# Performance work log

Hardware: AMD Instinct MI355X
Metric: run time of the kernel (lower is better)

## Reference

```python
import jax, jax.numpy as jnp
import numpy as np

B, HH, WW, C, HEADS = 8, 56, 56, 384, 6
DIM_OUT = 384


def _upsample2x_bilinear(x):
    # x: [..., m, n] -> [..., 2m, 2n]; matches torch F.interpolate bilinear align_corners=False
    m, n = x.shape[-2], x.shape[-1]
    def coords(inn):
        c = (jnp.arange(2 * inn) + 0.5) / 2.0 - 0.5
        c = jnp.clip(c, 0.0, inn - 1)
        i0 = jnp.floor(c).astype(jnp.int32)
        i1 = jnp.minimum(i0 + 1, inn - 1)
        return i0, i1, (c - i0).astype(x.dtype)
    i0, i1, wy = coords(m)
    j0, j1, wx = coords(n)
    rows = x[..., i0, :] * (1 - wy)[:, None] + x[..., i1, :] * wy[:, None]
    return rows[..., :, j0] * (1 - wx) + rows[..., :, j1] * wx


def setup_inputs() -> dict:
    key = jax.random.key(0)
    ks = jax.random.split(key, 12)
    inp = {
        'x': jax.random.normal(ks[0], (B, HH * WW, C), jnp.float32),
        'res_attn': jax.random.normal(ks[1], (B, HEADS, (HH // 4) * (WW // 4), (HH // 2) * (WW // 2)), jnp.float32),
        'conv_q_w': jax.random.normal(ks[2], (C, 1, 3, 3), jnp.float32) * 0.05,
        'ln_g': jnp.ones((C,), jnp.float32),
        'ln_b': jnp.zeros((C,), jnp.float32),
        'wq': jax.random.normal(ks[3], (DIM_OUT, C), jnp.float32) * 0.02,
        'wk': jax.random.normal(ks[4], (DIM_OUT, C), jnp.float32) * 0.02,
        'wv': jax.random.normal(ks[5], (DIM_OUT, C), jnp.float32) * 0.02,
        'w_proj': jax.random.normal(ks[6], (DIM_OUT, DIM_OUT), jnp.float32) * 0.02,
        'b_proj': jnp.zeros((DIM_OUT,), jnp.float32),
        'w_fuse': jax.random.normal(ks[7], (HEADS, 2 * HEADS, 1, 1), jnp.float32) * 0.1,
        'b_fuse': jnp.zeros((HEADS,), jnp.float32),
        'h': HH,
        'w': WW,
    }
    return inp


def reference(x, res_attn, conv_q_w, ln_g, ln_b, wq, wk, wv, w_proj, b_proj, w_fuse, b_fuse, h, w):
    Bz, _, Cc = x.shape
    heads = w_fuse.shape[0]
    xi = x.transpose(0, 2, 1).reshape(Bz, Cc, h, w)  # b c h w
    # conv_proj_q: depthwise conv k3 s2 p1 (no bias), then LayerNorm
    q = jax.lax.conv_general_dilated(
        xi, conv_q_w, (2, 2), ((1, 1), (1, 1)),
        dimension_numbers=('NCHW', 'OIHW', 'NCHW'), feature_group_count=Cc)
    hq, wq2 = q.shape[2], q.shape[3]
    q = q.reshape(Bz, Cc, hq * wq2).transpose(0, 2, 1)  # b t c
    mu = q.mean(-1, keepdims=True)
    var = ((q - mu) ** 2).mean(-1, keepdims=True)
    q = (q - mu) / jnp.sqrt(var + 1e-5) * ln_g + ln_b
    # conv_proj_k/v: avg pool k2 s2 p0
    kv = xi.reshape(Bz, Cc, h // 2, 2, w // 2, 2).mean(axis=(3, 5))
    kv = kv.reshape(Bz, Cc, (h // 2) * (w // 2)).transpose(0, 2, 1)  # b t c
    dim_out = wq.shape[0]
    dh = dim_out // heads
    def split(t):
        return t.reshape(Bz, t.shape[1], heads, dh).transpose(0, 2, 1, 3)
    qh = split(q @ wq.T)
    kh = split(kv @ wk.T)
    vh = split(kv @ wv.T)
    scale = dim_out ** -0.5
    attn_score = jnp.einsum('bhlk,bhtk->bhlt', qh, kh) * scale  # [B,H,L,T]
    sh, sw = h // 4, w // 4
    a = res_attn.shape[-1]
    rx = res_attn[:, :, :sh * sw, :]
    rx = rx.reshape(Bz * heads, sh * sw, a).transpose(0, 2, 1).reshape(Bz * heads, a, sh, sw)
    rx = _upsample2x_bilinear(rx)  # (b h) a 2sh 2sw
    rx = rx.reshape(Bz, heads, a, 4 * sh * sw).transpose(0, 1, 3, 2)  # b h L a
    cat = jnp.concatenate([attn_score, rx], axis=1)  # [B, 2H, L, T]
    attn_score = jnp.einsum('bclt,oc->bolt', cat, w_fuse[:, :, 0, 0]) + b_fuse[None, :, None, None]
    attn = jax.nn.softmax(attn_score, axis=-1)
    out = jnp.einsum('bhlt,bhtv->bhlv', attn, vh)
    out = out.transpose(0, 2, 1, 3).reshape(Bz, -1, dim_out)
    return out @ w_proj.T + b_proj
```

## Files before the change

### kernel.cpp

```cpp
#include <hip/hip_runtime.h>

typedef unsigned int uint;
typedef unsigned short ushort_t;
typedef short bf16x8 __attribute__((ext_vector_type(8)));
typedef float f32x4 __attribute__((ext_vector_type(4)));

__device__ __forceinline__ ushort_t f2bf(float f) {
  uint u = __builtin_bit_cast(uint, f);
  u += 0x7fffu + ((u >> 16) & 1u);
  return (ushort_t)(u >> 16);
}
__device__ __forceinline__ float bf2f(ushort_t s) {
  return __builtin_bit_cast(float, (uint)s << 16);
}
__device__ __forceinline__ float bflo(uint u) { return __builtin_bit_cast(float, u << 16); }
__device__ __forceinline__ float bfhi(uint u) { return __builtin_bit_cast(float, u & 0xffff0000u); }
__device__ __forceinline__ bf16x8 ld_frag(const ushort_t* p) {
  return __builtin_bit_cast(bf16x8, *(const uint4*)p);
}

__global__ __launch_bounds__(384) void k_prep(
    const float* __restrict__ x, const float* __restrict__ wc,
    const float* __restrict__ g, const float* __restrict__ bb,
    ushort_t* __restrict__ qout, ushort_t* __restrict__ kvout)
{
  const int b  = blockIdx.x / 784;
  const int t  = blockIdx.x % 784;
  const int oy = t / 28, ox = t % 28;
  const int c  = threadIdx.x;
  const float* xb = x + (size_t)b * 3136 * 384 + c;
  float tap[9];
  #pragma unroll
  for (int ky = 0; ky < 3; ky++) {
    const int iy = 2 * oy - 1 + ky;
    #pragma unroll
    for (int kx = 0; kx < 3; kx++) {
      const int ix = 2 * ox - 1 + kx;
      tap[ky * 3 + kx] = (iy >= 0 && iy < 56 && ix >= 0 && ix < 56)
                         ? xb[(size_t)(iy * 56 + ix) * 384] : 0.f;
    }
  }
  float acc = 0.f;
  #pragma unroll
  for (int k = 0; k < 9; k++) acc += wc[c * 9 + k] * tap[k];
  const float pool = (tap[4] + tap[5] + tap[7] + tap[8]) * 0.25f;

  float s = acc, s2 = acc * acc;
  #pragma unroll
  for (int off = 32; off >= 1; off >>= 1) {
    s  += __shfl_xor(s,  off);
    s2 += __shfl_xor(s2, off);
  }
  __shared__ float ps[6], ps2[6];
  if ((c & 63) == 0) { ps[c >> 6] = s; ps2[c >> 6] = s2; }
  __syncthreads();
  float S = 0.f, S2 = 0.f;
  #pragma unroll
  for (int i = 0; i < 6; i++) { S += ps[i]; S2 += ps2[i]; }
  const float mu  = S * (1.f / 384.f);
  const float var = S2 * (1.f / 384.f) - mu * mu;
  const float inv = rsqrtf(var + 1e-5f);
  const size_t o = ((size_t)b * 784 + t) * 384 + c;
  qout[o]  = f2bf((acc - mu) * inv * g[c] + bb[c]);
  kvout[o] = f2bf(pool);
}

__global__ __launch_bounds__(256) void k_wcvt(
    const float* __restrict__ a, const float* __restrict__ b,
    const float* __restrict__ c, const float* __restrict__ d,
    ushort_t* __restrict__ oa, ushort_t* __restrict__ ob,
    ushort_t* __restrict__ oc, ushort_t* __restrict__ od)
{
  const int i = blockIdx.x * 256 + threadIdx.x;
  if (i < 147456) {
    oa[i] = f2bf(a[i]); ob[i] = f2bf(b[i]);
    oc[i] = f2bf(c[i]); od[i] = f2bf(d[i]);
  }
}

__global__ __launch_bounds__(256) void k_rcmix(
    const float* __restrict__ ra, const float* __restrict__ w_fuse,
    ushort_t* __restrict__ RC)
{
  const int tid = threadIdx.x;
  const int b = blockIdx.x / 196, lc = blockIdx.x % 196;
  __shared__ float w2[36];
  if (tid < 36) w2[tid] = w_fuse[(tid / 6) * 12 + 6 + (tid % 6)];
  __syncthreads();
  const float* rab = ra + ((size_t)b * 6 * 196 + lc) * 784;
  ushort_t* RCb = RC + ((size_t)b * 6 * 196 + lc) * 784;
  for (int t = tid; t < 784; t += 256) {
    float U[6];
    #pragma unroll
    for (int c = 0; c < 6; c++) U[c] = rab[(size_t)c * 153664 + t];
    #pragma unroll
    for (int o = 0; o < 6; o++) {
      float v = 0.f;
      #pragma unroll
      for (int c = 0; c < 6; c++) v += w2[o * 6 + c] * U[c];
      RCb[(size_t)o * 153664 + t] = f2bf(v);
    }
  }
}

template<int MODE>
__global__ __launch_bounds__(256) void k_gemm(
    const ushort_t* __restrict__ X, const ushort_t* __restrict__ W,
    const float* __restrict__ bias, void* __restrict__ Y)
{
  __shared__ ushort_t As[128][40];
  __shared__ ushort_t Bs[128][40];
  const int tid = threadIdx.x, w = tid >> 6, lane = tid & 63;
  const int quad = lane >> 4, r = lane & 15;
  const int m0 = blockIdx.y * 128, n0 = blockIdx.x * 128;
  const int wm = w >> 1, wn = w & 1;
  const int lr = tid >> 2, lc = (tid & 3) << 3;
  const ushort_t* xp = X + (size_t)(m0 + lr) * 384 + lc;
  const ushort_t* wp = W + (size_t)(n0 + lr) * 384 + lc;
  f32x4 acc[4][4] = {};
  for (int k0 = 0; k0 < 384; k0 += 32) {
    __syncthreads();
    *(uint4*)&As[lr][lc]      = *(const uint4*)(xp + k0);
    *(uint4*)&As[lr + 64][lc] = *(const uint4*)(xp + (size_t)64 * 384 + k0);
    *(uint4*)&Bs[lr][lc]      = *(const uint4*)(wp + k0);
    *(uint4*)&Bs[lr + 64][lc] = *(const uint4*)(wp + (size_t)64 * 384 + k0);
    __syncthreads();
    bf16x8 af[4], bf_[4];
    #pragma unroll
    for (int mt = 0; mt < 4; mt++) af[mt]  = *(const bf16x8*)&As[wm * 64 + mt * 16 + r][quad * 8];
    #pragma unroll
    for (int nt = 0; nt < 4; nt++) bf_[nt] = *(const bf16x8*)&Bs[wn * 64 + nt * 16 + r][quad * 8];
    #pragma unroll
    for (int mt = 0; mt < 4; mt++)
      #pragma unroll
      for (int nt = 0; nt < 4; nt++)
        acc[mt][nt] = __builtin_amdgcn_mfma_f32_16x16x32_bf16(af[mt], bf_[nt], acc[mt][nt], 0, 0, 0);
  }
  #pragma unroll
  for (int mt = 0; mt < 4; mt++) {
    #pragma unroll
    for (int nt = 0; nt < 4; nt++) {
      #pragma unroll
      for (int i = 0; i < 4; i++) {
        const int row = m0 + wm * 64 + mt * 16 + quad * 4 + i;
        const int col = n0 + wn * 64 + nt * 16 + r;
        const float v = acc[mt][nt][i];
        if constexpr (MODE == 2) ((float*)Y)[(size_t)row * 384 + col] = v + bias[col];
        else                     ((ushort_t*)Y)[(size_t)row * 384 + col] = f2bf(v);
      }
    }
  }
}

__global__ __launch_bounds__(256) void k_gemmT(
    const ushort_t* __restrict__ W, const ushort_t* __restrict__ X,
    ushort_t* __restrict__ Vt)
{
  __shared__ ushort_t As[128][40];
  __shared__ ushort_t Bs[128][40];
  const int tid = threadIdx.x, w = tid >> 6, lane = tid & 63;
  const int quad = lane >> 4, r = lane & 15;
  const int m0 = blockIdx.y * 128, n0 = blockIdx.x * 128;
  const int wm = w >> 1, wn = w & 1;
  const int lr = tid >> 2, lc = (tid & 3) << 3;
  const ushort_t* ap = W + (size_t)(m0 + lr) * 384 + lc;
  const ushort_t* bp = X + (size_t)(n0 + lr) * 384 + lc;
  f32x4 acc[4][4] = {};
  for (int k0 = 0; k0 < 384; k0 += 32) {
    __syncthreads();
    *(uint4*)&As[lr][lc]      = *(const uint4*)(ap + k0);
    *(uint4*)&As[lr + 64][lc] = *(const uint4*)(ap + (size_t)64 * 384 + k0);
    *(uint4*)&Bs[lr][lc]      = *(const uint4*)(bp + k0);
    *(uint4*)&Bs[lr + 64][lc] = *(const uint4*)(bp + (size_t)64 * 384 + k0);
    __syncthreads();
    bf16x8 af[4], bf_[4];
    #pragma unroll
    for (int mt = 0; mt < 4; mt++) af[mt]  = *(const bf16x8*)&As[wm * 64 + mt * 16 + r][quad * 8];
    #pragma unroll
    for (int nt = 0; nt < 4; nt++) bf_[nt] = *(const bf16x8*)&Bs[wn * 64 + nt * 16 + r][quad * 8];
    #pragma unroll
    for (int mt = 0; mt < 4; mt++)
      #pragma unroll
      for (int nt = 0; nt < 4; nt++)
        acc[mt][nt] = __builtin_amdgcn_mfma_f32_16x16x32_bf16(af[mt], bf_[nt], acc[mt][nt], 0, 0, 0);
  }
  #pragma unroll
  for (int mt = 0; mt < 4; mt++) {
    #pragma unroll
    for (int nt = 0; nt < 4; nt++) {
      #pragma unroll
      for (int i = 0; i < 4; i++) {
        const int d   = m0 + wm * 64 + mt * 16 + quad * 4 + i;
        const int tok = n0 + wn * 64 + nt * 16 + r;
        const int b = tok / 784, tt = tok % 784;
        Vt[((size_t)b * 384 + d) * 784 + tt] = f2bf(acc[mt][nt][i]);
      }
    }
  }
}

__global__ __launch_bounds__(256, 3) void k_fattn(
    const ushort_t* __restrict__ Qb, const ushort_t* __restrict__ Kb,
    const ushort_t* __restrict__ Vt, const ushort_t* __restrict__ RC,
    const float* __restrict__ w_fuse, const float* __restrict__ b_fuse,
    float* __restrict__ Op, float2* __restrict__ MS)
{
  __shared__ char smem[27648];
  ushort_t* Ssc_ = (ushort_t*)smem;
  ushort_t* Pl_  = (ushort_t*)(smem + 13824);
  float*    stage = (float*)smem;
  #define SSC(h, l, t) Ssc_[(((h) * 16 + (l)) * 72) + (t)]
  #define PL(h, l, t)  Pl_[(((h) * 16 + (l)) * 72) + (t)]
  __shared__ float m_st[6][16], s_st[6][16], a_st[6][16];
  __shared__ float w1[36], bfu[6];

  const int tid  = threadIdx.x;
  const int w    = tid >> 6, lane = tid & 63;
  const int quad = lane >> 4, r = lane & 15;
  const int b    = blockIdx.x & 7;
  const int m0   = (blockIdx.x >> 3) * 16;
  const int s    = blockIdx.y;
  const int tile0 = (s == 0) ? 0 : (3 * s + 1);
  const int tileN = (s == 0) ? 4 : 3;
  const float scale = 0.05103103630798288f;

  if (tid < 36) w1[tid] = w_fuse[(tid / 6) * 12 + (tid % 6)] * scale;
  if (tid < 6)  bfu[tid] = b_fuse[tid];
  if (tid < 96) { (&m_st[0][0])[tid] = -1e30f; (&s_st[0][0])[tid] = 0.f; }

  const ushort_t* qrow = Qb + ((size_t)(b * 784 + m0 + r)) * 384 + quad * 8;
  bf16x8 qf[6][2];
  #pragma unroll
  for (int h = 0; h < 6; h++) {
    qf[h][0] = ld_frag(qrow + h * 64);
    qf[h][1] = ld_frag(qrow + h * 64 + 32);
  }

  const int bl_l = tid >> 4, tq = tid & 15;
  const int L = m0 + bl_l;
  const int Yc = L / 28, Xc = L % 28;
  const float cy = fminf(fmaxf((float)Yc * 0.5f - 0.25f, 0.f), 13.f);
  const float cx = fminf(fmaxf((float)Xc * 0.5f - 0.25f, 0.f), 13.f);
  const int y0 = (int)cy, y1 = min(y0 + 1, 13);
  const int x0 = (int)cx, x1 = min(x0 + 1, 13);
  const float fy = cy - (float)y0, fx = cx - (float)x0;
  const float w00 = (1.f - fy) * (1.f - fx), w01 = (1.f - fy) * fx;
  const float w10 = fy * (1.f - fx),         w11 = fy * fx;
  const int q00 = (y0 * 14 + x0) * 784, q01 = (y0 * 14 + x1) * 784;
  const int q10 = (y1 * 14 + x0) * 784, q11 = (y1 * 14 + x1) * 784;
  const ushort_t* RCb = RC + (size_t)b * 6 * 153664;

  const size_t kbase  = (size_t)b * 784 * 384;
  const size_t vtbase = (size_t)b * 384 * 784;

  f32x4 oacc[6] = {};

  for (int ii = 0; ii < tileN; ii++) {
    const int t0 = (tile0 + ii) * 64;

    {
      const int tA = min(t0 + w * 16 + r, 783);
      const ushort_t* krow = Kb + kbase + (size_t)tA * 384 + quad * 8;
      #pragma unroll
      for (int h = 0; h < 6; h++) {
        f32x4 sc = {};
        sc = __builtin_amdgcn_mfma_f32_16x16x32_bf16(qf[h][0], ld_frag(krow + h * 64),      sc, 0, 0, 0);
        sc = __builtin_amdgcn_mfma_f32_16x16x32_bf16(qf[h][1], ld_frag(krow + h * 64 + 32), sc, 0, 0, 0);
        #pragma unroll
        for (int i = 0; i < 4; i++)
          SSC(h, quad * 4 + i, w * 16 + r) = f2bf(sc[i]);
      }
    }
    __syncthreads();

    {
      const int t4 = t0 + tq * 4;
      float F[6][4];
      #pragma unroll
      for (int o = 0; o < 6; o++) {
        const ushort_t* rco = RCb + (size_t)o * 153664 + t4;
        const uint2 u00 = *(const uint2*)(rco + q00);
        const uint2 u01 = *(const uint2*)(rco + q01);
        const uint2 u10 = *(const uint2*)(rco + q10);
        const uint2 u11 = *(const uint2*)(rco + q11);
        F[o][0] = bfu[o] + w00 * bflo(u00.x) + w01 * bflo(u01.x) + w10 * bflo(u10.x) + w11 * bflo(u11.x);
        F[o][1] = bfu[o] + w00 * bfhi(u00.x) + w01 * bfhi(u01.x) + w10 * bfhi(u10.x) + w11 * bfhi(u11.x);
        F[o][2] = bfu[o] + w00 * bflo(u00.y) + w01 * bflo(u01.y) + w10 * bflo(u10.y) + w11 * bflo(u11.y);
        F[o][3] = bfu[o] + w00 * bfhi(u00.y) + w01 * bfhi(u01.y) + w10 * bfhi(u10.y) + w11 * bfhi(u11.y);
      }
      #pragma unroll
      for (int c = 0; c < 6; c++) {
        const uint2 sv = *(const uint2*)&SSC(c, bl_l, tq * 4);
        const float s0 = bflo(sv.x), s1 = bfhi(sv.x);
        const float s2 = bflo(sv.y), s3 = bfhi(sv.y);
        #pragma unroll
        for (int o = 0; o < 6; o++) {
          const float wv = w1[o * 6 + c];
          F[o][0] += wv * s0; F[o][1] += wv * s1;
          F[o][2] += wv * s2; F[o][3] += wv * s3;
        }
      }
      #pragma unroll
      for (int j = 0; j < 4; j++) {
        if (t4 + j >= 784) {
          #pragma unroll
          for (int o = 0; o < 6; o++) F[o][j] = -1e30f;
        }
      }
      #pragma unroll
      for (int o = 0; o < 6; o++) {
        float mx = fmaxf(fmaxf(F[o][0], F[o][1]), fmaxf(F[o][2], F[o][3]));
        #pragma unroll
        for (int off = 8; off >= 1; off >>= 1) mx = fmaxf(mx, __shfl_xor(mx, off));
        const float m_old = m_st[o][bl_l];
        const float nm = fmaxf(m_old, mx);
        const float al = __expf(m_old - nm);
        float p0 = __expf(F[o][0] - nm), p1 = __expf(F[o][1] - nm);
        float p2 = __expf(F[o][2] - nm), p3 = __expf(F[o][3] - nm);
        float sm = p0 + p1 + p2 + p3;
        #pragma unroll
        for (int off = 8; off >= 1; off >>= 1) sm += __shfl_xor(sm, off);
        const uint lo = (uint)f2bf(p0) | ((uint)f2bf(p1) << 16);
        const uint hi = (uint)f2bf(p2) | ((uint)f2bf(p3) << 16);
        *(uint2*)&PL(o, bl_l, tq * 4) = uint2{lo, hi};
        if (tq == 0) {
          m_st[o][bl_l] = nm;
          s_st[o][bl_l] = s_st[o][bl_l] * al + sm;
          a_st[o][bl_l] = al;
        }
      }
    }
    __syncthreads();

    #pragma unroll
    for (int o = 0; o < 6; o++) {
      const f32x4 al4 = *(const f32x4*)&a_st[o][quad * 4];
      oacc[o] *= al4;
      const bf16x8 pa0 = *(const bf16x8*)&PL(o, r, quad * 8);
      const bf16x8 pa1 = *(const bf16x8*)&PL(o, r, quad * 8 + 32);
      const ushort_t* vrow = Vt + vtbase + (size_t)(o * 64 + w * 16 + r) * 784 + t0 + quad * 8;
      oacc[o] = __builtin_amdgcn_mfma_f32_16x16x32_bf16(pa0, ld_frag(vrow),      oacc[o], 0, 0, 0);
      oacc[o] = __builtin_amdgcn_mfma_f32_16x16x32_bf16(pa1, ld_frag(vrow + 32), oacc[o], 0, 0, 0);
    }
    __syncthreads();
  }

  #pragma unroll
  for (int o = 0; o < 6; o++)
    #pragma unroll
    for (int i = 0; i < 4; i++)
      stage[(quad * 4 + i) * 392 + o * 64 + w * 16 + r] = oacc[o][i];
  __syncthreads();
  const size_t prow = (size_t)s * 6272 + (size_t)b * 784 + m0;
  #pragma unroll
  for (int j = 0; j < 6; j++) {
    const int idx = tid + j * 256;
    const int row = idx / 96, c4 = idx % 96;
    *(float4*)&Op[(prow + row) * 384 + c4 * 4] = *(const float4*)&stage[row * 392 + c4 * 4];
  }
  if (tid < 96) {
    const int l = tid / 6, o = tid % 6;
    MS[(prow + l) * 6 + o] = float2{m_st[o][l], s_st[o][l]};
  }
  #undef SSC
  #undef PL
}

__global__ __launch_bounds__(256) void k_comb(
    const float* __restrict__ Op, const float2* __restrict__ MS,
    ushort_t* __restrict__ O)
{
  const int idx = blockIdx.x * 256 + threadIdx.x;
  const int row = idx / 384, col = idx % 384, o = col >> 6;
  float2 ms[4];
  #pragma unroll
  for (int s = 0; s < 4; s++) ms[s] = MS[((size_t)s * 6272 + row) * 6 + o];
  float m = fmaxf(fmaxf(ms[0].x, ms[1].x), fmaxf(ms[2].x, ms[3].x));
  float S = 0.f, acc = 0.f;
  #pragma unroll
  for (int s = 0; s < 4; s++) {
    const float e = __expf(ms[s].x - m);
    S   += ms[s].y * e;
    acc += Op[((size_t)s * 6272 + row) * 384 + col] * e;
  }
  O[(size_t)row * 384 + col] = f2bf(acc / S);
}

extern "C" void kernel_launch(void* const* d_in, const int* in_sizes, int n_in,
                              void* d_out, int out_size, void* d_ws, size_t ws_size,
                              hipStream_t stream)
{
  const float* x        = (const float*)d_in[0];
  const float* res_attn = (const float*)d_in[1];
  const float* conv_w   = (const float*)d_in[2];
  const float* ln_g     = (const float*)d_in[3];
  const float* ln_b     = (const float*)d_in[4];
  const float* wq       = (const float*)d_in[5];
  const float* wk       = (const float*)d_in[6];
  const float* wv       = (const float*)d_in[7];
  const float* w_proj   = (const float*)d_in[8];
  const float* b_proj   = (const float*)d_in[9];
  const float* w_fuse   = (const float*)d_in[10];
  const float* b_fuse   = (const float*)d_in[11];
  float* out = (float*)d_out;

  const size_t NE  = (size_t)8 * 784 * 384;
  const size_t NW  = 147456;
  const size_t NRC = (size_t)8 * 6 * 196 * 784;
  ushort_t* q_ln_b = (ushort_t*)d_ws;
  ushort_t* kv_b   = q_ln_b + NE;
  ushort_t* Qb     = kv_b + NE;
  ushort_t* Kb     = Qb + NE;
  ushort_t* Vt     = Kb + NE;
  ushort_t* Opre   = Vt + NE + 64;
  ushort_t* wqb    = Opre + NE;
  ushort_t* wkb    = wqb + NW;
  ushort_t* wvb    = wkb + NW;
  ushort_t* wpb    = wvb + NW;
  ushort_t* RC     = wpb + NW;
  float*    Op     = (float*)(RC + NRC + 64);
  float2*   MS     = (float2*)(Op + 4 * NE);

  k_prep <<<dim3(8 * 784), dim3(384), 0, stream>>>(x, conv_w, ln_g, ln_b, q_ln_b, kv_b);
  k_wcvt <<<dim3(576),     dim3(256), 0, stream>>>(wq, wk, wv, w_proj, wqb, wkb, wvb, wpb);
  k_rcmix<<<dim3(8 * 196), dim3(256), 0, stream>>>(res_attn, w_fuse, RC);

  k_gemm<0><<<dim3(3, 49), dim3(256), 0, stream>>>(q_ln_b, wqb, nullptr, Qb);
  k_gemm<0><<<dim3(3, 49), dim3(256), 0, stream>>>(kv_b,   wkb, nullptr, Kb);
  k_gemmT  <<<dim3(49, 3), dim3(256), 0, stream>>>(wvb, kv_b, Vt);

  k_fattn<<<dim3(392, 4), dim3(256), 0, stream>>>(Qb, Kb, Vt, RC, w_fuse, b_fuse, Op, MS);
  k_comb <<<dim3(9408),   dim3(256), 0, stream>>>(Op, MS, Opre);

  k_gemm<2><<<dim3(3, 49), dim3(256), 0, stream>>>(Opre, wpb, b_proj, out);
}
```

Before: 354.2 us.

## Precompute upsampled residual mix and drop split-K attention combine

```diff
diff --git a/kernel.cpp b/kernel.cpp
--- a/kernel.cpp
+++ b/kernel.cpp
@@ -24,8 +24,8 @@
     const float* __restrict__ g, const float* __restrict__ bb,
     ushort_t* __restrict__ qout, ushort_t* __restrict__ kvout)
 {
-  const int b  = blockIdx.x / 784;
-  const int t  = blockIdx.x % 784;
+  const int b  = blockIdx.x & 7;
+  const int t  = blockIdx.x >> 3;
   const int oy = t / 28, ox = t % 28;
   const int c  = threadIdx.x;
   const float* xb = x + (size_t)b * 3136 * 384 + c;
@@ -78,27 +78,45 @@
   }
 }
 
-__global__ __launch_bounds__(256) void k_rcmix(
+__global__ __launch_bounds__(256) void k_resmix(
     const float* __restrict__ ra, const float* __restrict__ w_fuse,
-    ushort_t* __restrict__ RC)
+    const float* __restrict__ b_fuse, ushort_t* __restrict__ R)
 {
   const int tid = threadIdx.x;
-  const int b = blockIdx.x / 196, lc = blockIdx.x % 196;
-  __shared__ float w2[36];
+  const int b = blockIdx.x & 7, L = blockIdx.x >> 3;
+  __shared__ float w2[36], bfu[6];
   if (tid < 36) w2[tid] = w_fuse[(tid / 6) * 12 + 6 + (tid % 6)];
+  if (tid < 6)  bfu[tid] = b_fuse[tid];
   __syncthreads();
-  const float* rab = ra + ((size_t)b * 6 * 196 + lc) * 784;
-  ushort_t* RCb = RC + ((size_t)b * 6 * 196 + lc) * 784;
+
+  const int Yc = L / 28, Xc = L % 28;
+  const float cy = fminf(fmaxf((float)Yc * 0.5f - 0.25f, 0.f), 13.f);
+  const float cx = fminf(fmaxf((float)Xc * 0.5f - 0.25f, 0.f), 13.f);
+  const int y0 = (int)cy, y1 = min(y0 + 1, 13);
+  const int x0 = (int)cx, x1 = min(x0 + 1, 13);
+  const float fy = cy - (float)y0, fx = cx - (float)x0;
+  const float w00 = (1.f - fy) * (1.f - fx), w01 = (1.f - fy) * fx;
+  const float w10 = fy * (1.f - fx),         w11 = fy * fx;
+  const int p00 = (y0 * 14 + x0) * 784, p01 = (y0 * 14 + x1) * 784;
+  const int p10 = (y1 * 14 + x0) * 784, p11 = (y1 * 14 + x1) * 784;
+
+  const float* rab = ra + (size_t)b * 6 * 153664;
+  ushort_t* Rrow = R + ((size_t)(b * 784 + L) * 6) * 784;
+
   for (int t = tid; t < 784; t += 256) {
     float U[6];
     #pragma unroll
-    for (int c = 0; c < 6; c++) U[c] = rab[(size_t)c * 153664 + t];
+    for (int c = 0; c < 6; c++) {
+      const float* rc = rab + (size_t)c * 153664;
+      U[c] = w00 * rc[p00 + t] + w01 * rc[p01 + t]
+           + w10 * rc[p10 + t] + w11 * rc[p11 + t];
+    }
     #pragma unroll
     for (int o = 0; o < 6; o++) {
-      float v = 0.f;
+      float v = bfu[o];
       #pragma unroll
       for (int c = 0; c < 6; c++) v += w2[o * 6 + c] * U[c];
-      RCb[(size_t)o * 153664 + t] = f2bf(v);
+      Rrow[(size_t)o * 784 + t] = f2bf(v);
     }
   }
 }
@@ -199,36 +217,31 @@
   }
 }
 
-__global__ __launch_bounds__(256, 3) void k_fattn(
+__global__ __launch_bounds__(128, 2) void k_fattn(
     const ushort_t* __restrict__ Qb, const ushort_t* __restrict__ Kb,
-    const ushort_t* __restrict__ Vt, const ushort_t* __restrict__ RC,
-    const float* __restrict__ w_fuse, const float* __restrict__ b_fuse,
-    float* __restrict__ Op, float2* __restrict__ MS)
-{
-  __shared__ char smem[27648];
-  ushort_t* Ssc_ = (ushort_t*)smem;
-  ushort_t* Pl_  = (ushort_t*)(smem + 13824);
-  float*    stage = (float*)smem;
-  #define SSC(h, l, t) Ssc_[(((h) * 16 + (l)) * 72) + (t)]
-  #define PL(h, l, t)  Pl_[(((h) * 16 + (l)) * 72) + (t)]
-  __shared__ float m_st[6][16], s_st[6][16], a_st[6][16];
-  __shared__ float w1[36], bfu[6];
+    const ushort_t* __restrict__ Vt, const ushort_t* __restrict__ R,
+    const float* __restrict__ w_fuse, ushort_t* __restrict__ O)
+{
+  __shared__ ushort_t Ssc[6][16][72];
+  __shared__ ushort_t Pl[6][16][72];
+  __shared__ float m_st[6][8], s_st[6][8];
+  __shared__ float a_st[6][16];
+  __shared__ float w1[36];
 
   const int tid  = threadIdx.x;
   const int w    = tid >> 6, lane = tid & 63;
   const int quad = lane >> 4, r = lane & 15;
   const int b    = blockIdx.x & 7;
-  const int m0   = (blockIdx.x >> 3) * 16;
-  const int s    = blockIdx.y;
-  const int tile0 = (s == 0) ? 0 : (3 * s + 1);
-  const int tileN = (s == 0) ? 4 : 3;
+  const int m0   = (blockIdx.x >> 3) * 8;
   const float scale = 0.05103103630798288f;
 
   if (tid < 36) w1[tid] = w_fuse[(tid / 6) * 12 + (tid % 6)] * scale;
-  if (tid < 6)  bfu[tid] = b_fuse[tid];
-  if (tid < 96) { (&m_st[0][0])[tid] = -1e30f; (&s_st[0][0])[tid] = 0.f; }
-
-  const ushort_t* qrow = Qb + ((size_t)(b * 784 + m0 + r)) * 384 + quad * 8;
+  if (tid < 48) { (&m_st[0][0])[tid] = -1e30f; (&s_st[0][0])[tid] = 0.f; }
+  if (tid < 96) (&a_st[0][0])[tid] = 1.f;
+  for (int i = tid; i < 864; i += 128) ((uint4*)Pl)[i] = uint4{0u, 0u, 0u, 0u};
+
+  const int lq = min(m0 + r, 783);
+  const ushort_t* qrow = Qb + ((size_t)(b * 784 + lq)) * 384 + quad * 8;
   bf16x8 qf[6][2];
   #pragma unroll
   for (int h = 0; h < 6; h++) {
@@ -237,29 +250,25 @@
   }
 
   const int bl_l = tid >> 4, tq = tid & 15;
-  const int L = m0 + bl_l;
-  const int Yc = L / 28, Xc = L % 28;
-  const float cy = fminf(fmaxf((float)Yc * 0.5f - 0.25f, 0.f), 13.f);
-  const float cx = fminf(fmaxf((float)Xc * 0.5f - 0.25f, 0.f), 13.f);
-  const int y0 = (int)cy, y1 = min(y0 + 1, 13);
-  const int x0 = (int)cx, x1 = min(x0 + 1, 13);
-  const float fy = cy - (float)y0, fx = cx - (float)x0;
-  const float w00 = (1.f - fy) * (1.f - fx), w01 = (1.f - fy) * fx;
-  const float w10 = fy * (1.f - fx),         w11 = fy * fx;
-  const int q00 = (y0 * 14 + x0) * 784, q01 = (y0 * 14 + x1) * 784;
-  const int q10 = (y1 * 14 + x0) * 784, q11 = (y1 * 14 + x1) * 784;
-  const ushort_t* RCb = RC + (size_t)b * 6 * 153664;
+  const ushort_t* Rrow = R + ((size_t)(b * 784 + m0 + bl_l) * 6) * 784;
 
   const size_t kbase  = (size_t)b * 784 * 384;
   const size_t vtbase = (size_t)b * 384 * 784;
 
-  f32x4 oacc[6] = {};
-
-  for (int ii = 0; ii < tileN; ii++) {
-    const int t0 = (tile0 + ii) * 64;
-
-    {
-      const int tA = min(t0 + w * 16 + r, 783);
+  f32x4 oacc[6][2] = {};
+
+  for (int it = 0; it < 13; it++) {
+    const int t0 = it * 64;
+
+    const int t4 = t0 + tq * 4;
+    uint2 rv[6];
+    #pragma unroll
+    for (int o = 0; o < 6; o++)
+      rv[o] = *(const uint2*)(Rrow + (size_t)o * 784 + t4);
+
+    #pragma unroll
+    for (int sub = 0; sub < 2; sub++) {
+      const int tA = min(t0 + w * 32 + sub * 16 + r, 783);
       const ushort_t* krow = Kb + kbase + (size_t)tA * 384 + quad * 8;
       #pragma unroll
       for (int h = 0; h < 6; h++) {
@@ -268,29 +277,21 @@
         sc = __builtin_amdgcn_mfma_f32_16x16x32_bf16(qf[h][1], ld_frag(krow + h * 64 + 32), sc, 0, 0, 0);
         #pragma unroll
         for (int i = 0; i < 4; i++)
-          SSC(h, quad * 4 + i, w * 16 + r) = f2bf(sc[i]);
+          Ssc[h][quad * 4 + i][w * 32 + sub * 16 + r] = f2bf(sc[i]);
       }
     }
     __syncthreads();
 
     {
-      const int t4 = t0 + tq * 4;
       float F[6][4];
       #pragma unroll
       for (int o = 0; o < 6; o++) {
-        const ushort_t* rco = RCb + (size_t)o * 153664 + t4;
-        const uint2 u00 = *(const uint2*)(rco + q00);
-        const uint2 u01 = *(const uint2*)(rco + q01);
-        const uint2 u10 = *(const uint2*)(rco + q10);
-        const uint2 u11 = *(const uint2*)(rco + q11);
-        F[o][0] = bfu[o] + w00 * bflo(u00.x) + w01 * bflo(u01.x) + w10 * bflo(u10.x) + w11 * bflo(u11.x);
-        F[o][1] = bfu[o] + w00 * bfhi(u00.x) + w01 * bfhi(u01.x) + w10 * bfhi(u10.x) + w11 * bfhi(u11.x);
-        F[o][2] = bfu[o] + w00 * bflo(u00.y) + w01 * bflo(u01.y) + w10 * bflo(u10.y) + w11 * bflo(u11.y);
-        F[o][3] = bfu[o] + w00 * bfhi(u00.y) + w01 * bfhi(u01.y) + w10 * bfhi(u10.y) + w11 * bfhi(u11.y);
+        F[o][0] = bflo(rv[o].x); F[o][1] = bfhi(rv[o].x);
+        F[o][2] = bflo(rv[o].y); F[o][3] = bfhi(rv[o].y);
       }
       #pragma unroll
       for (int c = 0; c < 6; c++) {
-        const uint2 sv = *(const uint2*)&SSC(c, bl_l, tq * 4);
+        const uint2 sv = *(const uint2*)&Ssc[c][bl_l][tq * 4];
         const float s0 = bflo(sv.x), s1 = bfhi(sv.x);
         const float s2 = bflo(sv.y), s3 = bfhi(sv.y);
         #pragma unroll
@@ -322,7 +323,7 @@
         for (int off = 8; off >= 1; off >>= 1) sm += __shfl_xor(sm, off);
         const uint lo = (uint)f2bf(p0) | ((uint)f2bf(p1) << 16);
         const uint hi = (uint)f2bf(p2) | ((uint)f2bf(p3) << 16);
-        *(uint2*)&PL(o, bl_l, tq * 4) = uint2{lo, hi};
+        *(uint2*)&Pl[o][bl_l][tq * 4] = uint2{lo, hi};
         if (tq == 0) {
           m_st[o][bl_l] = nm;
           s_st[o][bl_l] = s_st[o][bl_l] * al + sm;
@@ -335,55 +336,33 @@
     #pragma unroll
     for (int o = 0; o < 6; o++) {
       const f32x4 al4 = *(const f32x4*)&a_st[o][quad * 4];
-      oacc[o] *= al4;
-      const bf16x8 pa0 = *(const bf16x8*)&PL(o, r, quad * 8);
-      const bf16x8 pa1 = *(const bf16x8*)&PL(o, r, quad * 8 + 32);
-      const ushort_t* vrow = Vt + vtbase + (size_t)(o * 64 + w * 16 + r) * 784 + t0 + quad * 8;
-      oacc[o] = __builtin_amdgcn_mfma_f32_16x16x32_bf16(pa0, ld_frag(vrow),      oacc[o], 0, 0, 0);
-      oacc[o] = __builtin_amdgcn_mfma_f32_16x16x32_bf16(pa1, ld_frag(vrow + 32), oacc[o], 0, 0, 0);
-    }
-    __syncthreads();
-  }
-
-  #pragma unroll
-  for (int o = 0; o < 6; o++)
-    #pragma unroll
-    for (int i = 0; i < 4; i++)
-      stage[(quad * 4 + i) * 392 + o * 64 + w * 16 + r] = oacc[o][i];
-  __syncthreads();
-  const size_t prow = (size_t)s * 6272 + (size_t)b * 784 + m0;
-  #pragma unroll
-  for (int j = 0; j < 6; j++) {
-    const int idx = tid + j * 256;
-    const int row = idx / 96, c4 = idx % 96;
-    *(float4*)&Op[(prow + row) * 384 + c4 * 4] = *(const float4*)&stage[row * 392 + c4 * 4];
-  }
-  if (tid < 96) {
-    const int l = tid / 6, o = tid % 6;
-    MS[(prow + l) * 6 + o] = float2{m_st[o][l], s_st[o][l]};
-  }
-  #undef SSC
-  #undef PL
-}
-
-__global__ __launch_bounds__(256) void k_comb(
-    const float* __restrict__ Op, const float2* __restrict__ MS,
-    ushort_t* __restrict__ O)
-{
-  const int idx = blockIdx.x * 256 + threadIdx.x;
-  const int row = idx / 384, col = idx % 384, o = col >> 6;
-  float2 ms[4];
-  #pragma unroll
-  for (int s = 0; s < 4; s++) ms[s] = MS[((size_t)s * 6272 + row) * 6 + o];
-  float m = fmaxf(fmaxf(ms[0].x, ms[1].x), fmaxf(ms[2].x, ms[3].x));
-  float S = 0.f, acc = 0.f;
-  #pragma unroll
-  for (int s = 0; s < 4; s++) {
-    const float e = __expf(ms[s].x - m);
-    S   += ms[s].y * e;
-    acc += Op[((size_t)s * 6272 + row) * 384 + col] * e;
-  }
-  O[(size_t)row * 384 + col] = f2bf(acc / S);
+      const bf16x8 pa0 = *(const bf16x8*)&Pl[o][r][quad * 8];
+      const bf16x8 pa1 = *(const bf16x8*)&Pl[o][r][quad * 8 + 32];
+      #pragma unroll
+      for (int sub = 0; sub < 2; sub++) {
+        const int d = o * 64 + (w * 2 + sub) * 16 + r;
+        const ushort_t* vrow = Vt + vtbase + (size_t)d * 784 + t0 + quad * 8;
+        oacc[o][sub] *= al4;
+        oacc[o][sub] = __builtin_amdgcn_mfma_f32_16x16x32_bf16(pa0, ld_frag(vrow),      oacc[o][sub], 0, 0, 0);
+        oacc[o][sub] = __builtin_amdgcn_mfma_f32_16x16x32_bf16(pa1, ld_frag(vrow + 32), oacc[o][sub], 0, 0, 0);
+      }
+    }
+  }
+
+  if (quad < 2) {
+    #pragma unroll
+    for (int o = 0; o < 6; o++) {
+      #pragma unroll
+      for (int i = 0; i < 4; i++) {
+        const int l = quad * 4 + i;
+        const float inv = 1.f / s_st[o][l];
+        const size_t rowbase = (size_t)(b * 784 + m0 + l) * 384;
+        #pragma unroll
+        for (int sub = 0; sub < 2; sub++)
+          O[rowbase + o * 64 + (w * 2 + sub) * 16 + r] = f2bf(oacc[o][sub][i] * inv);
+      }
+    }
+  }
 }
 
 extern "C" void kernel_launch(void* const* d_in, const int* in_sizes, int n_in,
@@ -404,9 +383,9 @@
   const float* b_fuse   = (const float*)d_in[11];
   float* out = (float*)d_out;
 
-  const size_t NE  = (size_t)8 * 784 * 384;
-  const size_t NW  = 147456;
-  const size_t NRC = (size_t)8 * 6 * 196 * 784;
+  const size_t NE = (size_t)8 * 784 * 384;
+  const size_t NW = 147456;
+  const size_t NR = (size_t)8 * 784 * 6 * 784;
   ushort_t* q_ln_b = (ushort_t*)d_ws;
   ushort_t* kv_b   = q_ln_b + NE;
   ushort_t* Qb     = kv_b + NE;
@@ -417,20 +396,17 @@
   ushort_t* wkb    = wqb + NW;
   ushort_t* wvb    = wkb + NW;
   ushort_t* wpb    = wvb + NW;
-  ushort_t* RC     = wpb + NW;
-  float*    Op     = (float*)(RC + NRC + 64);
-  float2*   MS     = (float2*)(Op + 4 * NE);
-
-  k_prep <<<dim3(8 * 784), dim3(384), 0, stream>>>(x, conv_w, ln_g, ln_b, q_ln_b, kv_b);
-  k_wcvt <<<dim3(576),     dim3(256), 0, stream>>>(wq, wk, wv, w_proj, wqb, wkb, wvb, wpb);
-  k_rcmix<<<dim3(8 * 196), dim3(256), 0, stream>>>(res_attn, w_fuse, RC);
+  ushort_t* R      = wpb + NW;
+
+  k_prep  <<<dim3(8 * 784), dim3(384), 0, stream>>>(x, conv_w, ln_g, ln_b, q_ln_b, kv_b);
+  k_wcvt  <<<dim3(576),     dim3(256), 0, stream>>>(wq, wk, wv, w_proj, wqb, wkb, wvb, wpb);
+  k_resmix<<<dim3(8 * 784), dim3(256), 0, stream>>>(res_attn, w_fuse, b_fuse, R);
 
   k_gemm<0><<<dim3(3, 49), dim3(256), 0, stream>>>(q_ln_b, wqb, nullptr, Qb);
   k_gemm<0><<<dim3(3, 49), dim3(256), 0, stream>>>(kv_b,   wkb, nullptr, Kb);
   k_gemmT  <<<dim3(49, 3), dim3(256), 0, stream>>>(wvb, kv_b, Vt);
 
-  k_fattn<<<dim3(392, 4), dim3(256), 0, stream>>>(Qb, Kb, Vt, RC, w_fuse, b_fuse, Op, MS);
-  k_comb <<<dim3(9408),   dim3(256), 0, stream>>>(Op, MS, Opre);
+  k_fattn<<<dim3(784), dim3(128), 0, stream>>>(Qb, Kb, Vt, R, w_fuse, Opre);
 
   k_gemm<2><<<dim3(3, 49), dim3(256), 0, stream>>>(Opre, wpb, b_proj, out);
 }
```

Result: faster. 338.8 us (-4.3%).
